# Kernel optimization log

Measured on AMD Instinct MI355X. Metric: run time of the kernel, lower is better.

## Reference

```python
import jax, jax.numpy as jnp
import numpy as np

B, S, D, H = 2, 2048, 1024, 16
DH = D // H  # 64


def setup_inputs() -> dict:
    key = jax.random.key(0)
    k1, k2, k3, k4 = jax.random.split(key, 4)
    x = jax.random.normal(k1, (B, S, D), dtype=jnp.float32)
    # causal mask: 0 => masked (matches mask==0 -> -inf in source)
    mask = jnp.tril(jnp.ones((S, S), dtype=jnp.int32))
    Wq = jax.random.normal(k2, (H, D, DH), dtype=jnp.float32) * (D ** -0.5)
    Wk = jax.random.normal(k3, (H, D, DH), dtype=jnp.float32) * (D ** -0.5)
    Wo = jax.random.normal(k4, (D, D), dtype=jnp.float32) * (D ** -0.5)
    bo = jnp.zeros((D,), dtype=jnp.float32)
    return {"x": x, "mask": mask, "Wq": Wq, "Wk": Wk, "Wo": Wo, "bo": bo}


def reference(x, mask, Wq, Wk, Wo, bo):
    # Per source: q = query(x), k = key(x), v = query(x)  (bug kept: v == q)
    q = jnp.einsum('bsd,hde->bhse', x, Wq)   # [B,H,S,DH]
    k = jnp.einsum('bsd,hde->bhse', x, Wk)   # [B,H,S,DH]
    # scale uses d_model (input dim), not d_head -- faithful to source
    scale = jnp.asarray(D, x.dtype) ** -0.5
    scores = jnp.einsum('bhse,bhte->bhst', q, k) * scale  # [B,H,S,S]
    neg_inf = jnp.asarray(float('-inf'), scores.dtype)
    scores = jnp.where(mask[None, None, :, :] == 0, neg_inf, scores)
    w = jax.nn.softmax(scores, axis=-1)
    attn = jnp.einsum('bhst,bhte->bhse', w, q)  # v == q
    # concat heads: head axis becomes contiguous feature blocks
    attn = attn.transpose(0, 2, 1, 3).reshape(B, S, D)
    return attn @ Wo + bo
```

## Files before the change

### kernel.cpp

```cpp
#include <hip/hip_runtime.h>
#include <hip/hip_bf16.h>

#define BQ 2
#define SQ 2048
#define DMODEL 1024
#define NH 16
#define DH 64
#define NQT (SQ / 64)

typedef __attribute__((ext_vector_type(8))) short bf16x8;
typedef __attribute__((ext_vector_type(4))) short bf16x4;
typedef __attribute__((ext_vector_type(4))) float f32x4;
typedef unsigned short u16;

__device__ __forceinline__ u16 f2b(float f) {
  __hip_bfloat16 h = __float2bfloat16(f);
  return *reinterpret_cast<u16*>(&h);
}

__device__ __forceinline__ unsigned packbf(float lo, float hi) {
  return ((unsigned)f2b(hi) << 16) | (unsigned)f2b(lo);
}

#define MFMA(a, b, c) __builtin_amdgcn_mfma_f32_16x16x32_bf16((a), (b), (c), 0, 0, 0)

__device__ __forceinline__ f32x4 mfma16(bf16x4 a, bf16x4 b, f32x4 c) {
  asm("v_mfma_f32_16x16x16_bf16 %0, %1, %2, %0" : "+v"(c) : "v"(a), "v"(b));
  return c;
}

__device__ __forceinline__ unsigned cvtpk(float lo, float hi) {
  unsigned r;
  asm("v_cvt_pk_bf16_f32 %0, %1, %2" : "=v"(r) : "v"(lo), "v"(hi));
  return r;
}

#define CS (0.03125f * 1.44269504088896f)


__global__ void cvt_x_kernel(const float* __restrict__ x, u16* __restrict__ xb, int n) {
  int i = blockIdx.x * blockDim.x + threadIdx.x;
  int stride = gridDim.x * blockDim.x;
  for (; i < n; i += stride) xb[i] = f2b(x[i]);
}

__global__ __launch_bounds__(256) void prep_w_kernel(
    const float* __restrict__ Wq, const float* __restrict__ Wk,
    const float* __restrict__ Wo,
    u16* __restrict__ WqT, u16* __restrict__ WkT, u16* __restrict__ WoT) {
  __shared__ alignas(16) u16 T[64][72];
  int xt = blockIdx.x, yt = blockIdx.y, z = blockIdx.z;
  int tid = threadIdx.x;
  if (z < 2) {
    const float* W = z ? Wk : Wq;
    u16* WT = z ? WkT : WqT;
    const float* src = W + ((size_t)yt * 1024 + xt * 64) * 64;
#pragma unroll
    for (int i = 0; i < 4; ++i) {
      int lin = tid + i * 256;
      int r = lin >> 4, c4 = (lin & 15) * 4;
      float4 v = *(const float4*)&src[(size_t)r * 64 + c4];
      *(unsigned*)&T[r][c4]     = packbf(v.x, v.y);
      *(unsigned*)&T[r][c4 + 2] = packbf(v.z, v.w);
    }
    __syncthreads();
#pragma unroll
    for (int i = 0; i < 2; ++i) {
      int lin = tid + i * 256;
      int e = lin >> 3, d8 = (lin & 7) * 8;
      u16 tmp[8];
#pragma unroll
      for (int j = 0; j < 8; ++j) tmp[j] = T[d8 + j][e];
      *(uint4*)&WT[((size_t)yt * 64 + e) * 1024 + xt * 64 + d8] = *(uint4*)tmp;
    }
  } else {
    const float* src = Wo + ((size_t)xt * 64) * 1024 + yt * 64;
#pragma unroll
    for (int i = 0; i < 4; ++i) {
      int lin = tid + i * 256;
      int r = lin >> 4, c4 = (lin & 15) * 4;
      float4 v = *(const float4*)&src[(size_t)r * 1024 + c4];
      *(unsigned*)&T[r][c4]     = packbf(v.x, v.y);
      *(unsigned*)&T[r][c4 + 2] = packbf(v.z, v.w);
    }
    __syncthreads();
#pragma unroll
    for (int i = 0; i < 2; ++i) {
      int lin = tid + i * 256;
      int n = lin >> 3, k8 = (lin & 7) * 8;
      u16 tmp[8];
#pragma unroll
      for (int j = 0; j < 8; ++j) tmp[j] = T[k8 + j][n];
      *(uint4*)&WoT[((size_t)yt * 64 + n) * 1024 + xt * 64 + k8] = *(uint4*)tmp;
    }
  }
}

__global__ __launch_bounds__(256) void transpose_q_kernel(
    const u16* __restrict__ Q, u16* __restrict__ QT) {
  __shared__ alignas(16) u16 T[64][72];
  int st = blockIdx.x, h = blockIdx.y, b = blockIdx.z;
  size_t hb = ((size_t)(b * NH + h)) * SQ * DH;
  int tid = threadIdx.x;
#pragma unroll
  for (int i2 = 0; i2 < 2; ++i2) {
    int c = tid + i2 * 256;
    int r = c >> 3, cc = (c & 7) * 8;
    *(uint4*)&T[r][cc] = *(const uint4*)&Q[hb + (size_t)(st * 64 + r) * DH + cc];
  }
  __syncthreads();
#pragma unroll
  for (int i2 = 0; i2 < 2; ++i2) {
    int c = tid + i2 * 256;
    int e = c >> 3, s8 = (c & 7) * 8;
    u16 tmp[8];
#pragma unroll
    for (int j = 0; j < 8; ++j) tmp[j] = T[s8 + j][e];
    *(uint4*)&QT[hb + (size_t)e * SQ + st * 64 + s8] = *(uint4*)tmp;
  }
}


__global__ __launch_bounds__(256) void proj_kernel(
    const u16* __restrict__ xb,
    const u16* __restrict__ Wcat,
    u16* __restrict__ Qb, u16* __restrict__ Kb) {
  __shared__ alignas(16) u16 Xs[64][72];
  __shared__ alignas(16) u16 Ws[64][72];
  int st = blockIdx.x, hy = blockIdx.y, b = blockIdx.z;
  int tid = threadIdx.x, w = tid >> 6, l = tid & 63;
  int lr = l & 15, lk = (l >> 4) * 8;
  int r0s = tid >> 3, cc0 = (tid & 7) * 8, r1s = r0s + 32;
  f32x4 acc[4] = {};
  const u16* Ab = xb + (size_t)(b * SQ + st * 64) * DMODEL;
  const u16* Wb = Wcat + (size_t)hy * DH * DMODEL;

  *(uint4*)&Xs[r0s][cc0] = *(const uint4*)&Ab[(size_t)r0s * DMODEL + cc0];
  *(uint4*)&Xs[r1s][cc0] = *(const uint4*)&Ab[(size_t)r1s * DMODEL + cc0];
  *(uint4*)&Ws[r0s][cc0] = *(const uint4*)&Wb[(size_t)r0s * DMODEL + cc0];
  *(uint4*)&Ws[r1s][cc0] = *(const uint4*)&Wb[(size_t)r1s * DMODEL + cc0];
  __syncthreads();

  uint4 xr0 = *(const uint4*)&Ab[(size_t)r0s * DMODEL + 64 + cc0];
  uint4 xr1 = *(const uint4*)&Ab[(size_t)r1s * DMODEL + 64 + cc0];
  uint4 wv0 = *(const uint4*)&Wb[(size_t)r0s * DMODEL + 64 + cc0];
  uint4 wv1 = *(const uint4*)&Wb[(size_t)r1s * DMODEL + 64 + cc0];

  for (int ks = 0; ks < 16; ++ks) {
#pragma unroll
    for (int kk = 0; kk < 2; ++kk) {
      bf16x8 a = *(const bf16x8*)&Xs[w * 16 + lr][kk * 32 + lk];
#pragma unroll
      for (int n = 0; n < 4; ++n) {
        bf16x8 bb = *(const bf16x8*)&Ws[n * 16 + lr][kk * 32 + lk];
        acc[n] = MFMA(a, bb, acc[n]);
      }
    }
    if (ks < 15) {
      __syncthreads();
      *(uint4*)&Xs[r0s][cc0] = xr0;
      *(uint4*)&Xs[r1s][cc0] = xr1;
      *(uint4*)&Ws[r0s][cc0] = wv0;
      *(uint4*)&Ws[r1s][cc0] = wv1;
      if (ks + 2 < 16) {
        int k0 = (ks + 2) * 64;
        xr0 = *(const uint4*)&Ab[(size_t)r0s * DMODEL + k0 + cc0];
        xr1 = *(const uint4*)&Ab[(size_t)r1s * DMODEL + k0 + cc0];
        wv0 = *(const uint4*)&Wb[(size_t)r0s * DMODEL + k0 + cc0];
        wv1 = *(const uint4*)&Wb[(size_t)r1s * DMODEL + k0 + cc0];
      }
      __syncthreads();
    }
  }

  bool isQ = (hy < NH);
  u16* dst = isQ ? Qb : Kb;
  float scale = isQ ? 1.0f : CS;
  int hh = hy & (NH - 1);
  size_t obase = ((size_t)(b * NH + hh) * SQ + st * 64) * DH;
  int r0 = w * 16 + ((l >> 4) << 2);
#pragma unroll
  for (int n = 0; n < 4; ++n)
#pragma unroll
    for (int r = 0; r < 4; ++r)
      dst[obase + (size_t)(r0 + r) * DH + n * 16 + lr] = f2b(acc[n][r] * scale);
}


__global__ __launch_bounds__(512) void attn_kernel(
    const u16* __restrict__ Qt,
    const u16* __restrict__ Kt,
    const u16* __restrict__ QTt,
    u16* __restrict__ Oc) {
  __shared__ alignas(16) u16 Ks[2][64][72];
  __shared__ alignas(16) u16 Vs[2][64][72];
  int bx = blockIdx.x, h = blockIdx.y, b = blockIdx.z;
  int tid = threadIdx.x, w = tid >> 6, l = tid & 63;
  int lr = l & 15, hi = l >> 4, lk = hi * 8;
  int qlo = bx, qhi = NQT - 1 - bx;
  int qtile = (w >> 2) ? qhi : qlo;
  int q0 = qtile * 64 + (w & 3) * 16;
  int jmax = qhi;
  size_t hb = ((size_t)(b * NH + h)) * SQ * DH;

  int r0s = tid >> 3, cc0 = (tid & 7) * 8;

  bf16x8 aq[2];
  {
    const u16* qrow = Qt + hb + (size_t)(q0 + lr) * DH;
    aq[0] = *(const bf16x8*)&qrow[lk];
    aq[1] = *(const bf16x8*)&qrow[32 + lk];
  }

  *(uint4*)&Ks[0][r0s][cc0] = *(const uint4*)&Kt[hb + (size_t)r0s * DH + cc0];
  *(uint4*)&Vs[0][r0s][cc0] = *(const uint4*)&QTt[hb + (size_t)r0s * SQ + cc0];
  __syncthreads();

  uint4 kreg = *(const uint4*)&Kt[hb + (size_t)(64 + r0s) * DH + cc0];
  uint4 vreg = *(const uint4*)&QTt[hb + (size_t)r0s * SQ + 64 + cc0];

  f32x4 acc_t[4] = {};
  float l_run = 0.f;
  int cur = 0;

  for (int j = 0; j <= jmax; ++j) {
    if (j <= qtile) {
      f32x4 s[4] = {};
#pragma unroll
      for (int kk = 0; kk < 2; ++kk)
#pragma unroll
        for (int n = 0; n < 4; ++n) {
          bf16x8 bk = *(const bf16x8*)&Ks[cur][n * 16 + lr][kk * 32 + lk];
          s[n] = MFMA(bk, aq[kk], s[n]);
        }

      if (j == qtile) {
        int qg = q0 + lr;
#pragma unroll
        for (int n = 0; n < 4; ++n) {
          int kbase = j * 64 + n * 16 + hi * 4;
#pragma unroll
          for (int r = 0; r < 4; ++r)
            s[n][r] = (kbase + r > qg) ? 0.f : exp2f(s[n][r]);
        }
      } else {
#pragma unroll
        for (int n = 0; n < 4; ++n)
#pragma unroll
          for (int r = 0; r < 4; ++r) s[n][r] = exp2f(s[n][r]);
      }

#pragma unroll
      for (int n = 0; n < 4; ++n)
        l_run += (s[n][0] + s[n][1]) + (s[n][2] + s[n][3]);

      bf16x4 pb[4];
#pragma unroll
      for (int n = 0; n < 4; ++n) {
        uint2 u;
        u.x = cvtpk(s[n][0], s[n][1]);
        u.y = cvtpk(s[n][2], s[n][3]);
        pb[n] = *(bf16x4*)&u;
      }

#pragma unroll
      for (int nv = 0; nv < 4; ++nv) {
        const u16* vrow = &Vs[cur][nv * 16 + lr][hi * 4];
#pragma unroll
        for (int nh = 0; nh < 4; ++nh) {
          bf16x4 va = *(const bf16x4*)&vrow[nh * 16];
          acc_t[nv] = mfma16(va, pb[nh], acc_t[nv]);
        }
      }
    }

    if (j < jmax) {
      *(uint4*)&Ks[cur ^ 1][r0s][cc0] = kreg;
      *(uint4*)&Vs[cur ^ 1][r0s][cc0] = vreg;
      if (j + 2 <= jmax) {
        kreg = *(const uint4*)&Kt[hb + (size_t)((j + 2) * 64 + r0s) * DH + cc0];
        vreg = *(const uint4*)&QTt[hb + (size_t)r0s * SQ + (j + 2) * 64 + cc0];
      }
      __syncthreads();
      cur ^= 1;
    }
  }

  l_run += __shfl_xor(l_run, 16, 64);
  l_run += __shfl_xor(l_run, 32, 64);
  float inv = 1.f / l_run;

  size_t rbase = ((size_t)b * SQ + q0 + lr) * DMODEL + h * DH;
#pragma unroll
  for (int nv = 0; nv < 4; ++nv) {
#pragma unroll
    for (int rp = 0; rp < 2; ++rp) {
      unsigned pw = cvtpk(acc_t[nv][2 * rp] * inv, acc_t[nv][2 * rp + 1] * inv);
      *(unsigned*)&Oc[rbase + nv * 16 + hi * 4 + 2 * rp] = pw;
    }
  }
}


__global__ __launch_bounds__(256) void outproj_kernel(
    const u16* __restrict__ Oc,
    const u16* __restrict__ WoT,
    const float* __restrict__ bo,
    float* __restrict__ out) {
  __shared__ alignas(16) u16 Xs[64][72];
  __shared__ alignas(16) u16 Ws[64][72];
  int rt = blockIdx.x, nt = blockIdx.y;
  int tid = threadIdx.x, w = tid >> 6, l = tid & 63;
  int lr = l & 15, lk = (l >> 4) * 8;
  int r0s = tid >> 3, cc0 = (tid & 7) * 8, r1s = r0s + 32;
  f32x4 acc[4] = {};
  const u16* Ab = Oc + (size_t)rt * 64 * DMODEL;
  const u16* Wb = WoT + (size_t)nt * 64 * DMODEL;

  *(uint4*)&Xs[r0s][cc0] = *(const uint4*)&Ab[(size_t)r0s * DMODEL + cc0];
  *(uint4*)&Xs[r1s][cc0] = *(const uint4*)&Ab[(size_t)r1s * DMODEL + cc0];
  *(uint4*)&Ws[r0s][cc0] = *(const uint4*)&Wb[(size_t)r0s * DMODEL + cc0];
  *(uint4*)&Ws[r1s][cc0] = *(const uint4*)&Wb[(size_t)r1s * DMODEL + cc0];
  __syncthreads();

  uint4 xr0 = *(const uint4*)&Ab[(size_t)r0s * DMODEL + 64 + cc0];
  uint4 xr1 = *(const uint4*)&Ab[(size_t)r1s * DMODEL + 64 + cc0];
  uint4 wv0 = *(const uint4*)&Wb[(size_t)r0s * DMODEL + 64 + cc0];
  uint4 wv1 = *(const uint4*)&Wb[(size_t)r1s * DMODEL + 64 + cc0];

  for (int ks = 0; ks < 16; ++ks) {
#pragma unroll
    for (int kk = 0; kk < 2; ++kk) {
      bf16x8 a = *(const bf16x8*)&Xs[w * 16 + lr][kk * 32 + lk];
#pragma unroll
      for (int n = 0; n < 4; ++n) {
        bf16x8 bb = *(const bf16x8*)&Ws[n * 16 + lr][kk * 32 + lk];
        acc[n] = MFMA(a, bb, acc[n]);
      }
    }
    if (ks < 15) {
      __syncthreads();
      *(uint4*)&Xs[r0s][cc0] = xr0;
      *(uint4*)&Xs[r1s][cc0] = xr1;
      *(uint4*)&Ws[r0s][cc0] = wv0;
      *(uint4*)&Ws[r1s][cc0] = wv1;
      if (ks + 2 < 16) {
        int k0 = (ks + 2) * 64;
        xr0 = *(const uint4*)&Ab[(size_t)r0s * DMODEL + k0 + cc0];
        xr1 = *(const uint4*)&Ab[(size_t)r1s * DMODEL + k0 + cc0];
        wv0 = *(const uint4*)&Wb[(size_t)r0s * DMODEL + k0 + cc0];
        wv1 = *(const uint4*)&Wb[(size_t)r1s * DMODEL + k0 + cc0];
      }
      __syncthreads();
    }
  }

  int r0 = w * 16 + ((l >> 4) << 2);
#pragma unroll
  for (int n = 0; n < 4; ++n) {
    int col = nt * 64 + n * 16 + lr;
    float bv = bo[col];
#pragma unroll
    for (int r = 0; r < 4; ++r)
      out[(size_t)(rt * 64 + r0 + r) * DMODEL + col] = acc[n][r] + bv;
  }
}


extern "C" void kernel_launch(void* const* d_in, const int* in_sizes, int n_in,
                              void* d_out, int out_size, void* d_ws, size_t ws_size,
                              hipStream_t stream) {
  const float* x  = (const float*)d_in[0];
  const float* Wq = (const float*)d_in[2];
  const float* Wk = (const float*)d_in[3];
  const float* Wo = (const float*)d_in[4];
  const float* bo = (const float*)d_in[5];
  float* out = (float*)d_out;

  char* ws = (char*)d_ws;
  u16* xb  = (u16*)ws;
  u16* WqT = xb + (size_t)BQ * SQ * DMODEL;
  u16* WkT = WqT + (size_t)NH * DH * DMODEL;
  u16* WoT = WkT + (size_t)NH * DH * DMODEL;
  u16* Qb  = WoT + (size_t)DMODEL * DMODEL;
  u16* Kb  = Qb + (size_t)BQ * NH * SQ * DH;
  u16* Ob  = Kb + (size_t)BQ * NH * SQ * DH;
  u16* QTb = xb;

  cvt_x_kernel<<<2048, 256, 0, stream>>>(x, xb, BQ * SQ * DMODEL);
  prep_w_kernel<<<dim3(16, 16, 3), 256, 0, stream>>>(Wq, Wk, Wo, WqT, WkT, WoT);

  proj_kernel<<<dim3(SQ / 64, 2 * NH, BQ), 256, 0, stream>>>(xb, WqT, Qb, Kb);
  transpose_q_kernel<<<dim3(SQ / 64, NH, BQ), 256, 0, stream>>>(Qb, QTb);
  attn_kernel<<<dim3(16, NH, BQ), 512, 0, stream>>>(Qb, Kb, QTb, Ob);
  outproj_kernel<<<dim3(BQ * SQ / 64, DMODEL / 64, 1), 256, 0, stream>>>(Ob, WoT, bo, out);
}
```

Measured before the change: 116.2 us.

## Fuse Q transpose into projection epilogue and remap causal attention tiles

The projection kernel now stages its output tile in shared memory, writes Q/K with coalesced 16-byte stores, and also writes the transposed Q directly. This removes the separate transpose launch when the workspace is large enough. The attention kernel's tile assignment changes from pairing a low and a high query tile to adjacent tile pairs, with the order reversed between batches to balance causal work. The cost is extra shared-memory passes and syncs in the projection epilogue, and a different load balance in attention.

```diff
diff --git a/kernel.cpp b/kernel.cpp
--- a/kernel.cpp
+++ b/kernel.cpp
@@ -124,12 +124,13 @@
 __global__ __launch_bounds__(256) void proj_kernel(
     const u16* __restrict__ xb,
     const u16* __restrict__ Wcat,
-    u16* __restrict__ Qb, u16* __restrict__ Kb) {
+    u16* __restrict__ Qb, u16* __restrict__ Kb,
+    u16* __restrict__ QT) {
   __shared__ alignas(16) u16 Xs[64][72];
   __shared__ alignas(16) u16 Ws[64][72];
   int st = blockIdx.x, hy = blockIdx.y, b = blockIdx.z;
   int tid = threadIdx.x, w = tid >> 6, l = tid & 63;
-  int lr = l & 15, lk = (l >> 4) * 8;
+  int lr = l & 15, hi = l >> 4, lk = hi * 8;
   int r0s = tid >> 3, cc0 = (tid & 7) * 8, r1s = r0s + 32;
   f32x4 acc[4] = {};
   const u16* Ab = xb + (size_t)(b * SQ + st * 64) * DMODEL;
@@ -174,16 +175,38 @@
   }
 
   bool isQ = (hy < NH);
-  u16* dst = isQ ? Qb : Kb;
   float scale = isQ ? 1.0f : CS;
   int hh = hy & (NH - 1);
-  size_t obase = ((size_t)(b * NH + hh) * SQ + st * 64) * DH;
-  int r0 = w * 16 + ((l >> 4) << 2);
+  size_t hbh = ((size_t)(b * NH + hh)) * SQ * DH;
+  size_t obase = hbh + (size_t)st * 64 * DH;
+  int r0 = w * 16 + (hi << 2);
+  u16 (*Cs)[72] = Xs;
+  __syncthreads();
 #pragma unroll
   for (int n = 0; n < 4; ++n)
 #pragma unroll
     for (int r = 0; r < 4; ++r)
-      dst[obase + (size_t)(r0 + r) * DH + n * 16 + lr] = f2b(acc[n][r] * scale);
+      Cs[r0 + r][n * 16 + lr] = f2b(acc[n][r] * scale);
+  __syncthreads();
+
+  u16* dst = isQ ? Qb : Kb;
+#pragma unroll
+  for (int i2 = 0; i2 < 2; ++i2) {
+    int lin = tid + i2 * 256;
+    int r = lin >> 3, c8 = (lin & 7) * 8;
+    *(uint4*)&dst[obase + (size_t)r * DH + c8] = *(const uint4*)&Cs[r][c8];
+  }
+  if (isQ && QT) {
+#pragma unroll
+    for (int i2 = 0; i2 < 2; ++i2) {
+      int lin = tid + i2 * 256;
+      int e = lin >> 3, s8 = (lin & 7) * 8;
+      u16 tmp[8];
+#pragma unroll
+      for (int j = 0; j < 8; ++j) tmp[j] = Cs[s8 + j][e];
+      *(uint4*)&QT[hbh + (size_t)e * SQ + st * 64 + s8] = *(uint4*)tmp;
+    }
+  }
 }
 
 
@@ -195,12 +218,12 @@
   __shared__ alignas(16) u16 Ks[2][64][72];
   __shared__ alignas(16) u16 Vs[2][64][72];
   int bx = blockIdx.x, h = blockIdx.y, b = blockIdx.z;
+  int p = b ? bx : (15 - bx);
   int tid = threadIdx.x, w = tid >> 6, l = tid & 63;
   int lr = l & 15, hi = l >> 4, lk = hi * 8;
-  int qlo = bx, qhi = NQT - 1 - bx;
-  int qtile = (w >> 2) ? qhi : qlo;
+  int qtile = 2 * p + (w >> 2);
   int q0 = qtile * 64 + (w & 3) * 16;
-  int jmax = qhi;
+  int jmax = 2 * p + 1;
   size_t hb = ((size_t)(b * NH + h)) * SQ * DH;
 
   int r0s = tid >> 3, cc0 = (tid & 7) * 8;
@@ -385,13 +408,19 @@
   u16* Qb  = WoT + (size_t)DMODEL * DMODEL;
   u16* Kb  = Qb + (size_t)BQ * NH * SQ * DH;
   u16* Ob  = Kb + (size_t)BQ * NH * SQ * DH;
-  u16* QTb = xb;
+  u16* QTnew = Ob + (size_t)BQ * SQ * DMODEL;
+
+  size_t need = ((size_t)QTnew - (size_t)ws) + (size_t)BQ * SQ * DMODEL * sizeof(u16);
+  bool fused = ws_size >= need;
+  u16* QTb = fused ? QTnew : xb;
 
   cvt_x_kernel<<<2048, 256, 0, stream>>>(x, xb, BQ * SQ * DMODEL);
   prep_w_kernel<<<dim3(16, 16, 3), 256, 0, stream>>>(Wq, Wk, Wo, WqT, WkT, WoT);
 
-  proj_kernel<<<dim3(SQ / 64, 2 * NH, BQ), 256, 0, stream>>>(xb, WqT, Qb, Kb);
-  transpose_q_kernel<<<dim3(SQ / 64, NH, BQ), 256, 0, stream>>>(Qb, QTb);
+  proj_kernel<<<dim3(SQ / 64, 2 * NH, BQ), 256, 0, stream>>>(
+      xb, WqT, Qb, Kb, fused ? QTb : (u16*)nullptr);
+  if (!fused)
+    transpose_q_kernel<<<dim3(SQ / 64, NH, BQ), 256, 0, stream>>>(Qb, QTb);
   attn_kernel<<<dim3(16, NH, BQ), 512, 0, stream>>>(Qb, Kb, QTb, Ob);
   outproj_kernel<<<dim3(BQ * SQ / 64, DMODEL / 64, 1), 256, 0, stream>>>(Ob, WoT, bo, out);
 }
```

Result: faster. 110.5 us (-4.9%).
